# Optimization experiments

Hardware: AMD Instinct MI355X
Metric: run time of the kernel (lower is better)

The kernel has to match this reference:

```python
import jax, jax.numpy as jnp
import numpy as np

IN_SIZE = 256
N_THETA = 180
GRID = int(np.ceil(np.sqrt(2.0) * IN_SIZE))  # 363, == detector size == it_size


def _ramp_filter(P):
    # f is the spatial-domain ramp filter impulse response (Ram-Lak)
    n = np.concatenate([np.arange(1, P / 2 + 1, 2), np.arange(P / 2 - 1, 0, -2)])
    f = np.zeros(P, np.float32)
    f[0] = 0.25
    f[1::2] = -1.0 / (np.pi * n) ** 2
    # torch code multiplies both re/im by the real part of fft(f): complex * real scalar
    return jnp.asarray(2.0 * np.real(np.fft.fft(f)), jnp.float32)  # [P]


def _apply_ramp(x):
    # x: [N,C,S,A]; FFT filter along detector axis (2) with zero padding
    S = x.shape[2]
    P = max(64, int(2 ** np.ceil(np.log2(2 * S))))
    xp = jnp.pad(x, ((0, 0), (0, 0), (0, P - S), (0, 0)))
    filt = _ramp_filter(P)  # [P]
    spec = jnp.fft.fft(xp, axis=2) * filt[:, None]
    return jnp.real(jnp.fft.ifft(spec, axis=2))[:, :, :S, :].astype(x.dtype)


def _polar_T(G):
    # T[a,i,j] = xgrid*cos(theta_a) - ygrid*sin(theta_a), grids via meshgrid(ij)
    unit = jnp.linspace(-1.0, 1.0, G, dtype=jnp.float32)
    yg, xg = jnp.meshgrid(unit, unit, indexing='ij')
    th = jnp.deg2rad(jnp.arange(N_THETA, dtype=jnp.float32))  # [A]
    return xg[None] * jnp.cos(th)[:, None, None] - yg[None] * jnp.sin(th)[:, None, None]  # [A,G,G]


def _backproject(sino, T):
    # sino: [N,C,S,A]; grid X coord = i*2/(A-1)-1 picks column a exactly
    # (align_corners=True), so bilinear reduces to 1D lerp along the detector.
    N, C, S, A = sino.shape
    G = T.shape[1]
    pos = (T + 1.0) * (S - 1) / 2.0  # [A,G,G] fractional detector index
    i0 = jnp.floor(pos)
    w = (pos - i0).reshape(A, -1)  # [A,G*G]
    i0i = i0.astype(jnp.int32)
    i1i = i0i + 1
    ok0 = ((i0i >= 0) & (i0i < S)).reshape(A, -1)  # zeros padding outside
    ok1 = ((i1i >= 0) & (i1i < S)).reshape(A, -1)
    i0c = jnp.clip(i0i, 0, S - 1).reshape(A, -1)
    i1c = jnp.clip(i1i, 0, S - 1).reshape(A, -1)
    st = jnp.moveaxis(sino, 3, 2)  # [N,C,A,S]
    v0 = jnp.take_along_axis(st, i0c[None, None], axis=3)  # [N,C,A,G*G]
    v1 = jnp.take_along_axis(st, i1c[None, None], axis=3)
    w0 = jnp.where(ok0, 1.0 - w, 0.0)[None, None]
    w1 = jnp.where(ok1, w, 0.0)[None, None]
    reco = (v0 * w0 + v1 * w1).sum(axis=2)  # sum over angles
    return reco.reshape(N, C, G, G)


def setup_inputs() -> dict:
    key = jax.random.key(0)
    x = jax.random.normal(key, (4, 1, GRID, N_THETA), dtype=jnp.float32)
    return {"x": x}


def reference(x) -> jnp.ndarray:
    # filtered backprojection (inverse Radon), circle=False
    x = _apply_ramp(x)
    T = _polar_T(GRID)
    reco = _backproject(x, T)  # [N,C,G,G]
    # crop back to in_size x in_size (negative padding in torch code)
    W, G = IN_SIZE, GRID
    pad = G - W
    pad_before = (W + pad) // 2 - W // 2
    reco = reco[:, :, pad_before:G - (pad - pad_before), pad_before:G - (pad - pad_before)]
    return reco * (jnp.pi / (2.0 * N_THETA))
```

## Files before the change

kernel.cpp:

```cpp
#include <hip/hip_runtime.h>

#define S_DIM 363
#define S_P   368
#define A_DIM 180
#define OUT_W 256
#define F_PI 3.14159265358979323846f

typedef float    f4 __attribute__((ext_vector_type(4)));
typedef _Float16 h4 __attribute__((ext_vector_type(4)));
union HU  { uint2 u; h4 h; };
union HU2 { uint4 u; struct { h4 lo; h4 hi; } h; };

__device__ uint4 g_pair[A_DIM * S_P];

__global__ __launch_bounds__(384) void iradon_filter_kernel(
        const float* __restrict__ x) {
    __shared__ f4    xs4[S_DIM];
    __shared__ float wt[182];
    __shared__ h4    ys[366];

    const int a   = blockIdx.x;
    const int tid = threadIdx.x;

    if (tid < S_DIM) {
        f4 v;
        v.x = x[(0 * S_DIM + tid) * A_DIM + a];
        v.y = x[(1 * S_DIM + tid) * A_DIM + a];
        v.z = x[(2 * S_DIM + tid) * A_DIM + a];
        v.w = x[(3 * S_DIM + tid) * A_DIM + a];
        xs4[tid] = v;
    }
    if (tid < 182) {
        float d = (float)(2 * tid + 1);
        wt[tid] = -2.0f / (F_PI * F_PI * d * d);
    }
    if (tid == 363) ys[0]   = (h4)(_Float16)0.0f;
    if (tid == 364) ys[364] = (h4)(_Float16)0.0f;
    __syncthreads();

    if (tid < S_DIM) {
        f4 acc = 0.5f * xs4[tid];
        const int s0 = 1 - (tid & 1);
        #pragma unroll 4
        for (int s = s0; s < S_DIM; s += 2) {
            int d = s - tid; d = (d < 0) ? -d : d;
            float w = wt[d >> 1];
            acc += w * xs4[s];
        }
        ys[1 + tid] = __builtin_convertvector(acc, h4);
    }
    __syncthreads();

    if (tid < 364) {
        HU2 p;
        p.h.lo = ys[tid];
        p.h.hi = ys[tid + 1];
        g_pair[a * S_P + tid] = p.u;
    }
}

__global__ __launch_bounds__(256) void iradon_backproject_kernel(
        float* __restrict__ out) {
    __shared__ float cs[A_DIM];
    __shared__ float sn[A_DIM];
    __shared__ f4 red[256];

    const int tid = threadIdx.x;
    if (tid < A_DIM) {
        float th = (float)tid * (F_PI / 180.0f);
        cs[tid] = cosf(th);
        sn[tid] = sinf(th);
    }
    __syncthreads();

    const int px = tid & 63;
    const int q  = tid >> 6;
    const int tj = px & 31;
    const int ti = px >> 5;
    const int j  = blockIdx.x * 32 + tj;
    const int i  = blockIdx.y * 2 + ti;

    const float jj  = (float)(j - 128);
    const float nii = (float)(128 - i);

    f4 acc = (f4)0.0f;
    const int a0 = q * 45;
    #pragma unroll 3
    for (int m = 0; m < 45; ++m) {
        const int a = a0 + m;
        const float c = cs[a];
        const float s = sn[a];
        float pos = fmaf(jj, c, fmaf(nii, s, 181.0f));
        float f   = floorf(pos);
        int   k1  = (int)f + 1;
        float w1  = pos - f;
        float w0  = 1.0f - w1;
        HU2 v; v.u = g_pair[a * S_P + k1];
        acc.x = fmaf((float)v.h.lo.x, w0, fmaf((float)v.h.hi.x, w1, acc.x));
        acc.y = fmaf((float)v.h.lo.y, w0, fmaf((float)v.h.hi.y, w1, acc.y));
        acc.z = fmaf((float)v.h.lo.z, w0, fmaf((float)v.h.hi.z, w1, acc.z));
        acc.w = fmaf((float)v.h.lo.w, w0, fmaf((float)v.h.hi.w, w1, acc.w));
    }

    red[tid] = acc;
    __syncthreads();

    if (tid < 64) {
        f4 r = red[tid] + red[tid + 64] + red[tid + 128] + red[tid + 192];
        r *= (F_PI / 360.0f);
        const int jo = blockIdx.x * 32 + (tid & 31);
        const int io = blockIdx.y * 2 + (tid >> 5);
        const size_t p = (size_t)io * OUT_W + jo;
        out[p]              = r.x;
        out[p +     65536]  = r.y;
        out[p + 2 * 65536]  = r.z;
        out[p + 3 * 65536]  = r.w;
    }
}

extern "C" void kernel_launch(void* const* d_in, const int* in_sizes, int n_in,
                              void* d_out, int out_size, void* d_ws, size_t ws_size,
                              hipStream_t stream) {
    const float* x = (const float*)d_in[0];
    float* out = (float*)d_out;

    iradon_filter_kernel<<<dim3(A_DIM), 384, 0, stream>>>(x);
    iradon_backproject_kernel<<<dim3(OUT_W / 32, OUT_W / 2, 1), 256, 0, stream>>>(out);
}
```

Before: 73.49 us.

## Store single fp16 sinogram rows and use 64x1 pixel tiles in backprojection

The filter kernel now writes each filtered sample once as a 4-channel fp16 value straight to global memory. It no longer stages through shared memory and writes duplicated neighbour pairs. The backprojection kernel issues two 8-byte loads per angle instead of one 16-byte pair load, and each block now covers a 64x1 pixel strip instead of 32x2. This halves the sinogram footprint and removes a sync in the filter kernel, at the cost of twice as many gather instructions in the hot loop.

```diff
diff --git a/kernel.cpp b/kernel.cpp
--- a/kernel.cpp
+++ b/kernel.cpp
@@ -8,16 +8,14 @@
 
 typedef float    f4 __attribute__((ext_vector_type(4)));
 typedef _Float16 h4 __attribute__((ext_vector_type(4)));
-union HU  { uint2 u; h4 h; };
-union HU2 { uint4 u; struct { h4 lo; h4 hi; } h; };
+union HU { uint2 u; h4 h; };
 
-__device__ uint4 g_pair[A_DIM * S_P];
+__device__ uint2 g_sino[A_DIM * S_P];
 
 __global__ __launch_bounds__(384) void iradon_filter_kernel(
         const float* __restrict__ x) {
     __shared__ f4    xs4[S_DIM];
     __shared__ float wt[182];
-    __shared__ h4    ys[366];
 
     const int a   = blockIdx.x;
     const int tid = threadIdx.x;
@@ -34,8 +32,6 @@
         float d = (float)(2 * tid + 1);
         wt[tid] = -2.0f / (F_PI * F_PI * d * d);
     }
-    if (tid == 363) ys[0]   = (h4)(_Float16)0.0f;
-    if (tid == 364) ys[364] = (h4)(_Float16)0.0f;
     __syncthreads();
 
     if (tid < S_DIM) {
@@ -47,16 +43,11 @@
             float w = wt[d >> 1];
             acc += w * xs4[s];
         }
-        ys[1 + tid] = __builtin_convertvector(acc, h4);
+        HU r; r.h = __builtin_convertvector(acc, h4);
+        g_sino[a * S_P + 1 + tid] = r.u;
     }
-    __syncthreads();
-
-    if (tid < 364) {
-        HU2 p;
-        p.h.lo = ys[tid];
-        p.h.hi = ys[tid + 1];
-        g_pair[a * S_P + tid] = p.u;
-    }
+    if (tid == 363) { HU z; z.u.x = 0u; z.u.y = 0u; g_sino[a * S_P + 0]   = z.u; }
+    if (tid == 364) { HU z; z.u.x = 0u; z.u.y = 0u; g_sino[a * S_P + 364] = z.u; }
 }
 
 __global__ __launch_bounds__(256) void iradon_backproject_kernel(
@@ -75,10 +66,8 @@
 
     const int px = tid & 63;
     const int q  = tid >> 6;
-    const int tj = px & 31;
-    const int ti = px >> 5;
-    const int j  = blockIdx.x * 32 + tj;
-    const int i  = blockIdx.y * 2 + ti;
+    const int j  = blockIdx.x * 64 + px;
+    const int i  = blockIdx.y;
 
     const float jj  = (float)(j - 128);
     const float nii = (float)(128 - i);
@@ -95,11 +84,14 @@
         int   k1  = (int)f + 1;
         float w1  = pos - f;
         float w0  = 1.0f - w1;
-        HU2 v; v.u = g_pair[a * S_P + k1];
-        acc.x = fmaf((float)v.h.lo.x, w0, fmaf((float)v.h.hi.x, w1, acc.x));
-        acc.y = fmaf((float)v.h.lo.y, w0, fmaf((float)v.h.hi.y, w1, acc.y));
-        acc.z = fmaf((float)v.h.lo.z, w0, fmaf((float)v.h.hi.z, w1, acc.z));
-        acc.w = fmaf((float)v.h.lo.w, w0, fmaf((float)v.h.hi.w, w1, acc.w));
+        const uint2* __restrict__ row = g_sino + a * S_P;
+        HU lo, hi;
+        lo.u = row[k1];
+        hi.u = row[k1 + 1];
+        acc.x = fmaf((float)lo.h.x, w0, fmaf((float)hi.h.x, w1, acc.x));
+        acc.y = fmaf((float)lo.h.y, w0, fmaf((float)hi.h.y, w1, acc.y));
+        acc.z = fmaf((float)lo.h.z, w0, fmaf((float)hi.h.z, w1, acc.z));
+        acc.w = fmaf((float)lo.h.w, w0, fmaf((float)hi.h.w, w1, acc.w));
     }
 
     red[tid] = acc;
@@ -108,9 +100,8 @@
     if (tid < 64) {
         f4 r = red[tid] + red[tid + 64] + red[tid + 128] + red[tid + 192];
         r *= (F_PI / 360.0f);
-        const int jo = blockIdx.x * 32 + (tid & 31);
-        const int io = blockIdx.y * 2 + (tid >> 5);
-        const size_t p = (size_t)io * OUT_W + jo;
+        const int jo   = blockIdx.x * 64 + tid;
+        const size_t p = (size_t)blockIdx.y * OUT_W + jo;
         out[p]              = r.x;
         out[p +     65536]  = r.y;
         out[p + 2 * 65536]  = r.z;
@@ -125,5 +116,5 @@
     float* out = (float*)d_out;
 
     iradon_filter_kernel<<<dim3(A_DIM), 384, 0, stream>>>(x);
-    iradon_backproject_kernel<<<dim3(OUT_W / 32, OUT_W / 2, 1), 256, 0, stream>>>(out);
+    iradon_backproject_kernel<<<dim3(4, OUT_W), 256, 0, stream>>>(out);
 }
```

Measured after the change: 72.87 us. Within noise of the previous version (-0.8%).
